# Optimization experiments

Measured on AMD Instinct MI355X. Metric: run time of the kernel, lower is better.

## Reference

```python
import jax, jax.numpy as jnp
import numpy as np

C = 16          # scalar multiplicity of Rs_hidden = [(16, 0)]
NB = 10         # number_of_basis
H = 12          # radial MLP hidden size
MAX_R = 10.0
CENTERS = jnp.linspace(0.0, MAX_R, NB)
SIGMA = 0.8 * (MAX_R / (NB - 1))
GAUSS_NORM = 1.423085244900308   # e3nn GaussianRadialModel basis normalizer
Y0 = 1.0 / (2.0 * np.sqrt(np.pi))  # Y_{l=0} spherical harmonic constant


def setup_inputs() -> dict:
    key = jax.random.key(0)
    ks = jax.random.split(key, 9)
    z, n1, n2 = 4, 192, 192
    return {
        'input1': jax.random.normal(ks[0], (z, n1, C), jnp.float32),
        'input2': jax.random.normal(ks[1], (z, n2, C), jnp.float32),
        'xyz1': jax.random.normal(ks[2], (z, n1, 3), jnp.float32),
        'xyz2': jax.random.normal(ks[3], (z, n2, 3), jnp.float32),
        'mask': jax.random.randint(ks[4], (z, n1 + n2), 0, 2),
        'W_rad1': jax.random.normal(ks[5], (NB, H), jnp.float32),
        'W_rad_out': jax.random.normal(ks[6], (H, C * C), jnp.float32),
        'W_fc3': jax.random.normal(ks[7], (C, C), jnp.float32),
        'W_fc2': jax.random.normal(ks[8], (C, 1), jnp.float32),
    }


def _normalize(x, eps=1e-6):
    # torch .std defaults to unbiased (ddof=1)
    mean = x.mean(-1, keepdims=True)
    std = jnp.std(x, axis=-1, keepdims=True, ddof=1)
    return (x - mean) / (std + eps)


def reference(input1, input2, xyz1, xyz2, mask, W_rad1, W_rad_out, W_fc3, W_fc2):
    x = jnp.concatenate([input1, input2], axis=1)    # [z, n, C]
    xyz = jnp.concatenate([xyz1, xyz2], axis=1)      # [z, n, 3]
    z, n = x.shape[0], x.shape[1]

    # pairwise distances (eps keeps sqrt grad finite on the diagonal)
    diff = xyz[:, :, None, :] - xyz[:, None, :, :]   # [z, n, n, 3]
    d = jnp.sqrt(jnp.sum(diff * diff, axis=-1) + 1e-12)  # [z, n, n]

    # Gaussian radial basis + weight-normalized FC radial model (swish act)
    basis = jnp.exp(-jnp.square((d[..., None] - CENTERS) / SIGMA)) / GAUSS_NORM  # [z,n,n,NB]
    hmid = jax.nn.silu(basis @ W_rad1 / np.sqrt(NB))          # [z, n, n, H]
    R = hmid @ W_rad_out / np.sqrt(H)                         # [z, n, n, C*C]

    # l=0 TFN kernel: radial weights * Y_0 (trivial Clebsch-Gordan for scalars)
    K = R.reshape(z, n, n, C, C) * Y0                         # [z, a, b, i, j]
    y = jnp.einsum('zabij,zbj->zai', K, x)                    # [z, n, C]

    # Norm(Rs_hidden): per-irrep L2 norm; for scalars it's |x|
    y = jnp.abs(y)
    y = jnp.where(mask[..., None] == 0, 0.0, y)

    s = _normalize(jnp.sum(y, axis=1))                        # [z, C]
    h3 = jax.nn.leaky_relu(s @ W_fc3 / np.sqrt(C))            # fc3 + leaky_relu
    o = h3 @ W_fc2 / np.sqrt(C)                               # fc2
    return jax.nn.sigmoid(o).reshape(-1)                      # [z]
```

## Files before the change

### kernel.cpp

```cpp
#include <hip/hip_runtime.h>
#include <math.h>

#define Z     4
#define N1    192
#define NN    384
#define C     16
#define NB    10
#define H     12
#define ATILE 4
#define NAT   (NN / ATILE)
#define SPLIT 6

__device__ __forceinline__ float3 load_xyz(const float* __restrict__ xyz1,
                                           const float* __restrict__ xyz2,
                                           int z, int node) {
    const float* p = (node < N1) ? (xyz1 + (z * N1 + node) * 3)
                                 : (xyz2 + (z * N1 + (node - N1)) * 3);
    return make_float3(p[0], p[1], p[2]);
}

__global__ void k1_precompute_T(const float* __restrict__ in1,
                                const float* __restrict__ in2,
                                const float* __restrict__ Wro,
                                float* __restrict__ T) {
    const int bid = blockIdx.x;
    const int z = bid / NN, b = bid % NN;
    const int t = threadIdx.x;

    __shared__ float xl[C];
    if (t < C) {
        const float* xp = (b < N1) ? (in1 + (z * N1 + b) * C)
                                   : (in2 + (z * N1 + (b - N1)) * C);
        xl[t] = xp[t];
    }
    __syncthreads();

    const int h = t >> 4, i = t & 15;
    const float* w = Wro + h * (C * C) + i * C;
    float acc = 0.0f;
    #pragma unroll
    for (int j = 0; j < C; ++j) acc += w[j] * xl[j];

    const float scale = 0.28209479177387814f * 0.2886751345948129f;
    T[bid * (H * C) + t] = acc * scale;
}

__global__ __launch_bounds__(128, 4) void k2_pairs(const float* __restrict__ xyz1,
                                                   const float* __restrict__ xyz2,
                                                   const float* __restrict__ Wr1,
                                                   const float* __restrict__ T,
                                                   float* __restrict__ partial) {
    const int bid = blockIdx.x;
    const int sp  = bid % SPLIT;
    const int za  = bid / SPLIT;
    const int z   = za / NAT, at = za % NAT;
    const int a0  = at * ATILE;
    const int tid = threadIdx.x;
    const int lane = tid & 63, wv = tid >> 6;
    const int b = sp * 64 + lane;

    __shared__ float W1s[NB * H];
    __shared__ float red[2][32];
    if (tid < NB * H)
        W1s[tid] = Wr1[tid] * (0.31622776601683794f * 0.7027283689263438f);
    __syncthreads();

    const float3 pb = load_xyz(xyz1, xyz2, z, b);
    const float invSigma = 1.125f;

    float hm[ATILE][H];
    #pragma unroll
    for (int aa = 0; aa < ATILE; ++aa) {
        const float3 pa = load_xyz(xyz1, xyz2, z, a0 + aa);
        const float dx = pa.x - pb.x, dy = pa.y - pb.y, dz = pa.z - pb.z;
        const float d = sqrtf(dx * dx + dy * dy + dz * dz + 1e-12f);

        float acc[H];
        #pragma unroll
        for (int h = 0; h < H; ++h) acc[h] = 0.0f;
        #pragma unroll
        for (int k = 0; k < NB; ++k) {
            const float u = (d - (float)k * (10.0f / 9.0f)) * invSigma;
            const float e = __expf(-u * u);
            #pragma unroll
            for (int h = 0; h < H; ++h) acc[h] += e * W1s[k * H + h];
        }
        #pragma unroll
        for (int h = 0; h < H; ++h)
            hm[aa][h] = acc[h] / (1.0f + __expf(-acc[h]));
    }

    float v[ATILE * 8];
    #pragma unroll
    for (int p = 0; p < ATILE * 8; ++p) v[p] = 0.0f;

    const float4* tp = (const float4*)(T + (z * NN + b) * (H * C)) + wv * 2;
    #pragma unroll
    for (int h = 0; h < H; ++h) {
        const float4 t0 = tp[h * 4 + 0];
        const float4 t1 = tp[h * 4 + 1];
        #pragma unroll
        for (int aa = 0; aa < ATILE; ++aa) {
            const float f = hm[aa][h];
            const int o = aa * 8;
            v[o + 0] += f * t0.x;  v[o + 1] += f * t0.y;
            v[o + 2] += f * t0.z;  v[o + 3] += f * t0.w;
            v[o + 4] += f * t1.x;  v[o + 5] += f * t1.y;
            v[o + 6] += f * t1.z;  v[o + 7] += f * t1.w;
        }
    }

    #pragma unroll
    for (int k = 0; k < 5; ++k) {
        const int m = 16 >> k;
        const int bsel = (lane >> k) & 1;
        #pragma unroll
        for (int j = 0; j < m; ++j) {
            const float lo = v[j], hi = v[m + j];
            const float sendv = bsel ? lo : hi;
            const float recv = __shfl_xor(sendv, 1 << k, 64);
            v[j] = (bsel ? hi : lo) + recv;
        }
    }
    {
        const float recv = __shfl_xor(v[0], 32, 64);
        v[0] += recv;
    }
    const int l = lane & 31;
    const int pos = ((l & 1) << 4) | ((l & 2) << 2) | (l & 4) |
                    ((l & 8) >> 2) | ((l & 16) >> 4);
    if (lane < 32) red[wv][pos] = v[0];
    __syncthreads();

    if (tid < 64) {
        const int a_off = tid >> 4, i = tid & 15;
        const float val = (i < 8) ? red[0][a_off * 8 + i]
                                  : red[1][a_off * 8 + (i - 8)];
        partial[bid * 64 + tid] = val;
    }
}

__global__ __launch_bounds__(256) void k3_head(const float* __restrict__ partial,
                                               const int* __restrict__ mask,
                                               const float* __restrict__ Wfc3,
                                               const float* __restrict__ Wfc2,
                                               float* __restrict__ out) {
    const int z = blockIdx.x;
    const int t = threadIdx.x;
    const int i = t & 15, ch = t >> 4;

    __shared__ float red[16][17];
    __shared__ float sv[C];

    float acc = 0.0f;
    #pragma unroll
    for (int r = 0; r < 24; ++r) {
        const int a  = ch * 24 + r;
        const int at = a >> 2, t2 = a & 3;
        const int base = ((z * NAT + at) * SPLIT) * 64 + t2 * 16 + i;
        float val = 0.0f;
        #pragma unroll
        for (int s = 0; s < SPLIT; ++s) val += partial[base + s * 64];
        val = fabsf(val);
        if (mask[z * NN + a] != 0) acc += val;
    }
    red[ch][i] = acc;
    __syncthreads();
    if (t < C) {
        float s = 0.0f;
        #pragma unroll
        for (int c2 = 0; c2 < 16; ++c2) s += red[c2][t];
        sv[t] = s;
    }
    __syncthreads();

    if (t == 0) {
        float v[C];
        float mean = 0.0f;
        #pragma unroll
        for (int q = 0; q < C; ++q) { v[q] = sv[q]; mean += v[q]; }
        mean *= (1.0f / C);
        float var = 0.0f;
        #pragma unroll
        for (int q = 0; q < C; ++q) { const float d = v[q] - mean; var += d * d; }
        const float sd = sqrtf(var / (float)(C - 1)) + 1e-6f;
        #pragma unroll
        for (int q = 0; q < C; ++q) v[q] = (v[q] - mean) / sd;

        float o = 0.0f;
        #pragma unroll
        for (int k = 0; k < C; ++k) {
            float h3 = 0.0f;
            #pragma unroll
            for (int q = 0; q < C; ++q) h3 += v[q] * Wfc3[q * C + k];
            h3 *= 0.25f;
            h3 = (h3 > 0.0f) ? h3 : 0.01f * h3;
            o += h3 * Wfc2[k];
        }
        o *= 0.25f;
        out[z] = 1.0f / (1.0f + __expf(-o));
    }
}

extern "C" void kernel_launch(void* const* d_in, const int* in_sizes, int n_in,
                              void* d_out, int out_size, void* d_ws, size_t ws_size,
                              hipStream_t stream) {
    const float* in1  = (const float*)d_in[0];
    const float* in2  = (const float*)d_in[1];
    const float* xyz1 = (const float*)d_in[2];
    const float* xyz2 = (const float*)d_in[3];
    const int*   mask = (const int*)d_in[4];
    const float* Wr1  = (const float*)d_in[5];
    const float* Wro  = (const float*)d_in[6];
    const float* Wfc3 = (const float*)d_in[7];
    const float* Wfc2 = (const float*)d_in[8];
    float* out = (float*)d_out;

    float* T       = (float*)d_ws;
    float* partial = T + Z * NN * H * C;

    k1_precompute_T<<<Z * NN, 192, 0, stream>>>(in1, in2, Wro, T);
    k2_pairs<<<Z * NAT * SPLIT, 128, 0, stream>>>(xyz1, xyz2, Wr1, T, partial);
    k3_head<<<Z, 256, 0, stream>>>(partial, mask, Wfc3, Wfc2, out);
}
```

Before: 115.7 us.

## Transpose T to channel-major layout for coalesced loads; reorder radial basis loop

T is now stored with the node index b innermost, so lanes of a wavefront (consecutive b) read consecutive addresses instead of strided float4 rows, which makes the T loads coalesced. The Gaussian basis loop is restructured so the outer loop runs over basis index k, with W1 weights fetched from shared memory as float4 once per k and reused across all four a-rows. The cost is more scalar load instructions (96 scalar loads replacing 24 float4 loads) and the strided writes in k1.

```diff
diff --git a/kernel.cpp b/kernel.cpp
--- a/kernel.cpp
+++ b/kernel.cpp
@@ -42,7 +42,7 @@
     for (int j = 0; j < C; ++j) acc += w[j] * xl[j];
 
     const float scale = 0.28209479177387814f * 0.2886751345948129f;
-    T[bid * (H * C) + t] = acc * scale;
+    T[((z * H + h) * C + i) * NN + b] = acc * scale;
 }
 
 __global__ __launch_bounds__(128, 4) void k2_pairs(const float* __restrict__ xyz1,
@@ -68,45 +68,58 @@
     const float3 pb = load_xyz(xyz1, xyz2, z, b);
     const float invSigma = 1.125f;
 
-    float hm[ATILE][H];
+    float dd[ATILE];
     #pragma unroll
     for (int aa = 0; aa < ATILE; ++aa) {
         const float3 pa = load_xyz(xyz1, xyz2, z, a0 + aa);
         const float dx = pa.x - pb.x, dy = pa.y - pb.y, dz = pa.z - pb.z;
-        const float d = sqrtf(dx * dx + dy * dy + dz * dz + 1e-12f);
-
-        float acc[H];
-        #pragma unroll
-        for (int h = 0; h < H; ++h) acc[h] = 0.0f;
-        #pragma unroll
-        for (int k = 0; k < NB; ++k) {
-            const float u = (d - (float)k * (10.0f / 9.0f)) * invSigma;
+        dd[aa] = sqrtf(dx * dx + dy * dy + dz * dz + 1e-12f);
+    }
+
+    float acc[ATILE][H];
+    #pragma unroll
+    for (int aa = 0; aa < ATILE; ++aa)
+        #pragma unroll
+        for (int h = 0; h < H; ++h) acc[aa][h] = 0.0f;
+
+    #pragma unroll
+    for (int k = 0; k < NB; ++k) {
+        const float4 w0 = *(const float4*)&W1s[k * H + 0];
+        const float4 w1 = *(const float4*)&W1s[k * H + 4];
+        const float4 w2 = *(const float4*)&W1s[k * H + 8];
+        const float ck = (float)k * (10.0f / 9.0f);
+        #pragma unroll
+        for (int aa = 0; aa < ATILE; ++aa) {
+            const float u = (dd[aa] - ck) * invSigma;
             const float e = __expf(-u * u);
+            acc[aa][0]  += e * w0.x;  acc[aa][1]  += e * w0.y;
+            acc[aa][2]  += e * w0.z;  acc[aa][3]  += e * w0.w;
+            acc[aa][4]  += e * w1.x;  acc[aa][5]  += e * w1.y;
+            acc[aa][6]  += e * w1.z;  acc[aa][7]  += e * w1.w;
+            acc[aa][8]  += e * w2.x;  acc[aa][9]  += e * w2.y;
+            acc[aa][10] += e * w2.z;  acc[aa][11] += e * w2.w;
+        }
+    }
+    float hm[ATILE][H];
+    #pragma unroll
+    for (int aa = 0; aa < ATILE; ++aa)
+        #pragma unroll
+        for (int h = 0; h < H; ++h)
+            hm[aa][h] = acc[aa][h] / (1.0f + __expf(-acc[aa][h]));
+
+    float v[ATILE * 8];
+    #pragma unroll
+    for (int p = 0; p < ATILE * 8; ++p) v[p] = 0.0f;
+
+    const float* tb = T + ((z * H) * C + wv * 8) * NN + b;
+    #pragma unroll
+    for (int h = 0; h < H; ++h) {
+        #pragma unroll
+        for (int io = 0; io < 8; ++io) {
+            const float tval = tb[(h * C + io) * NN];
             #pragma unroll
-            for (int h = 0; h < H; ++h) acc[h] += e * W1s[k * H + h];
-        }
-        #pragma unroll
-        for (int h = 0; h < H; ++h)
-            hm[aa][h] = acc[h] / (1.0f + __expf(-acc[h]));
-    }
-
-    float v[ATILE * 8];
-    #pragma unroll
-    for (int p = 0; p < ATILE * 8; ++p) v[p] = 0.0f;
-
-    const float4* tp = (const float4*)(T + (z * NN + b) * (H * C)) + wv * 2;
-    #pragma unroll
-    for (int h = 0; h < H; ++h) {
-        const float4 t0 = tp[h * 4 + 0];
-        const float4 t1 = tp[h * 4 + 1];
-        #pragma unroll
-        for (int aa = 0; aa < ATILE; ++aa) {
-            const float f = hm[aa][h];
-            const int o = aa * 8;
-            v[o + 0] += f * t0.x;  v[o + 1] += f * t0.y;
-            v[o + 2] += f * t0.z;  v[o + 3] += f * t0.w;
-            v[o + 4] += f * t1.x;  v[o + 5] += f * t1.y;
-            v[o + 6] += f * t1.z;  v[o + 7] += f * t1.w;
+            for (int aa = 0; aa < ATILE; ++aa)
+                v[aa * 8 + io] += hm[aa][h] * tval;
         }
     }
 
```

After: 100.2 us. -13.4%, faster.
